# Kernel tuning notes

Measured on AMD Instinct MI355X. Metric: run time of the kernel, lower is better.

The kernel has to match this reference:

```python
import jax, jax.numpy as jnp
import numpy as np

D_K = 128

def setup_inputs() -> dict:
    key = jax.random.key(0)
    k1, k2, k3 = jax.random.split(key, 3)
    q = jax.random.normal(k1, (8192, D_K), dtype=jnp.float32)
    k = jax.random.normal(k2, (8192, D_K), dtype=jnp.float32)
    v = jax.random.normal(k3, (8192, D_K), dtype=jnp.float32)
    return {"q": q, "k": k, "v": v}

def reference(q, k, v):
    # scores: [S_q, S_k]
    scores = jnp.einsum('qd,kd->qk', q, k) / jnp.sqrt(jnp.float32(D_K))
    attn = jax.nn.softmax(scores, axis=-1)  # softmax over keys (torch default last dim)
    return jnp.einsum('qk,kd->qd', attn, v)
```

## Files before the change

### kernel.cpp

```cpp
#include <hip/hip_runtime.h>
#include <math.h>


typedef _Float16 f16x8 __attribute__((ext_vector_type(8)));
typedef float    f32x16 __attribute__((ext_vector_type(16)));

constexpr int S_LEN = 8192;
constexpr int D_K   = 128;
constexpr int NSLICE = 8;
constexpr int ITERS2 = (S_LEN / NSLICE) / 64;

constexpr size_t WS_L_OFF = 0;
constexpr size_t KV_OFF   = 262144;
constexpr size_t PART_OFF = KV_OFF + (size_t)256 * 16384;
constexpr size_t WS_NEED  = PART_OFF + (size_t)7 * S_LEN * D_K * 4;

#define CSCALE (0.08838834764831845f * 1.44269504088896340736f)

union UH8 { _Float16 h[8]; uint4 q; f16x8 v; };
union UF4 { unsigned u[4]; uint4 q; f16x8 v; };

__device__ inline void async16(const uint4* g, uint4* l) {
  __builtin_amdgcn_global_load_lds(
      (const __attribute__((address_space(1))) unsigned int*)g,
      (__attribute__((address_space(3))) unsigned int*)l, 16, 0, 0);
}

template <bool ZOUT>
__global__ __launch_bounds__(512) void attn_prep(const float* __restrict__ K,
                                                 const float* __restrict__ V,
                                                 float* __restrict__ out,
                                                 char* __restrict__ ws) {
  const int t = blockIdx.x * 512 + threadIdx.x;
  uint4* KVg = (uint4*)(ws + KV_OFF);
  if (t < 131072) {
    int kt = t >> 9, idx = t & 511;
    int lane = idx & 63, s = idx >> 6;
    int key = kt * 32 + (lane & 31);
    int d0  = s * 16 + (lane >> 5) * 8;
    const float4* src = (const float4*)(K + (size_t)key * D_K + d0);
    float4 a = src[0], b = src[1];
    float f[8] = {a.x, a.y, a.z, a.w, b.x, b.y, b.z, b.w};
    UH8 h;
    #pragma unroll
    for (int j = 0; j < 8; ++j) h.h[j] = (_Float16)f[j];
    KVg[(size_t)kt * 1024 + idx] = h.q;
  } else if (t < 262144) {
    int g = t - 131072;
    int kt = g >> 9, idx = g & 511;
    int lane = idx & 63, c = (idx >> 6) & 3, kstep = idx >> 8;
    int d  = c * 32 + (lane & 31);
    int kb = kt * 32 + kstep * 16 + (lane >> 5) * 8;
    UH8 h;
    #pragma unroll
    for (int j = 0; j < 8; ++j) h.h[j] = (_Float16)V[(size_t)(kb + j) * D_K + d];
    KVg[(size_t)kt * 1024 + 512 + idx] = h.q;
  } else if (ZOUT && t < 327680) {
    int i = t - 262144;
    float4 z = make_float4(0.f, 0.f, 0.f, 0.f);
    float4* o4 = (float4*)out;
    #pragma unroll
    for (int j = 0; j < 4; ++j) o4[(size_t)i * 4 + j] = z;
  } else if (ZOUT && t < 329728) {
    int i = t - 327680;
    ((float4*)(ws + WS_L_OFF))[i] = make_float4(0.f, 0.f, 0.f, 0.f);
  }
}

__device__ inline void softmax32(const f32x16& Sa, const f32x16& Sb, int lhalf,
                                 float& lsum, UF4& A0, UF4& A1) {
  unsigned pk[8];
  #pragma unroll
  for (int i = 0; i < 8; ++i) {
    float p0 = __builtin_amdgcn_exp2f(Sa[2 * i]     + Sb[2 * i]);
    float p1 = __builtin_amdgcn_exp2f(Sa[2 * i + 1] + Sb[2 * i + 1]);
    lsum += p0 + p1;
    pk[i] = __builtin_bit_cast(unsigned, __builtin_amdgcn_cvt_pkrtz(p0, p1));
  }
  unsigned s0 = __shfl_xor(pk[0], 32), s1 = __shfl_xor(pk[1], 32);
  unsigned s2 = __shfl_xor(pk[2], 32), s3 = __shfl_xor(pk[3], 32);
  unsigned s4 = __shfl_xor(pk[4], 32), s5 = __shfl_xor(pk[5], 32);
  unsigned s6 = __shfl_xor(pk[6], 32), s7 = __shfl_xor(pk[7], 32);
  A0.u[0] = lhalf ? s2 : pk[0];
  A0.u[1] = lhalf ? s3 : pk[1];
  A0.u[2] = lhalf ? pk[2] : s0;
  A0.u[3] = lhalf ? pk[3] : s1;
  A1.u[0] = lhalf ? s6 : pk[4];
  A1.u[1] = lhalf ? s7 : pk[5];
  A1.u[2] = lhalf ? pk[6] : s4;
  A1.u[3] = lhalf ? pk[7] : s5;
}

__device__ inline void pv8(const UF4& A0, const UF4& A1, const f16x8* vf,
                           f32x16* O) {
  #pragma unroll
  for (int kstep = 0; kstep < 2; ++kstep) {
    f16x8 pf = kstep ? A1.v : A0.v;
    O[0] = __builtin_amdgcn_mfma_f32_32x32x16_f16(pf, vf[kstep * 4 + 0], O[0], 0, 0, 0);
    O[1] = __builtin_amdgcn_mfma_f32_32x32x16_f16(pf, vf[kstep * 4 + 1], O[1], 0, 0, 0);
    O[2] = __builtin_amdgcn_mfma_f32_32x32x16_f16(pf, vf[kstep * 4 + 2], O[2], 0, 0, 0);
    O[3] = __builtin_amdgcn_mfma_f32_32x32x16_f16(pf, vf[kstep * 4 + 3], O[3], 0, 0, 0);
  }
}

template <bool PARTIAL>
__global__ __launch_bounds__(128, 1)
void attn_main(const float* __restrict__ Qg, float* __restrict__ out,
               char* __restrict__ ws) {
  __shared__ uint4 KV[2][2048];

  const int tid   = threadIdx.x;
  const int wave  = tid >> 6;
  const int lane  = tid & 63;
  const int lrow  = lane & 31;
  const int lhalf = lane >> 5;

  const int blk = blockIdx.x;
  const int ks  = blk & 7;
  const int qb  = blk >> 3;
  const int qw  = qb * 128 + wave * 64;

  float* ws_l = (float*)(ws + WS_L_OFF);

  f16x8 qf[2][8];
  #pragma unroll
  for (int qt = 0; qt < 2; ++qt) {
    const int q = qw + qt * 32 + lrow;
    #pragma unroll
    for (int s = 0; s < 8; ++s) {
      const float4* src = (const float4*)(Qg + (size_t)q * D_K + s * 16 + lhalf * 8);
      float4 a = src[0], b = src[1];
      float f[8] = {a.x, a.y, a.z, a.w, b.x, b.y, b.z, b.w};
      UH8 h;
      #pragma unroll
      for (int j = 0; j < 8; ++j) h.h[j] = (_Float16)(f[j] * CSCALE);
      qf[qt][s] = h.v;
    }
  }

  f32x16 O0[4] = {f32x16{}, f32x16{}, f32x16{}, f32x16{}};
  f32x16 O1[4] = {f32x16{}, f32x16{}, f32x16{}, f32x16{}};
  float ls0 = 0.f, ls1 = 0.f;

  const uint4* KVg = (const uint4*)(ws + KV_OFF);

  {
    const size_t base = (size_t)ks * 32768;
    #pragma unroll
    for (int i = 0; i < 16; ++i)
      async16(KVg + base + i * 128 + tid, &KV[0][i * 128 + tid]);
  }

  for (int it = 0; it < ITERS2; ++it) {
    const int buf = it & 1;
    __syncthreads();

    if (it + 1 < ITERS2) {
      const size_t base = (size_t)ks * 32768 + (size_t)(it + 1) * 2048;
      #pragma unroll
      for (int i = 0; i < 16; ++i)
        async16(KVg + base + i * 128 + tid, &KV[buf ^ 1][i * 128 + tid]);
    }

    #pragma unroll
    for (int st = 0; st < 2; ++st) {
      const uint4* sub = &KV[buf][st * 1024];

      f16x8 kf[8];
      #pragma unroll
      for (int s = 0; s < 8; ++s)
        kf[s] = __builtin_bit_cast(f16x8, sub[s * 64 + lane]);

      f32x16 Sa0{}, Sb0{}, Sa1{}, Sb1{};
      #pragma unroll
      for (int s = 0; s < 4; ++s) {
        Sa0 = __builtin_amdgcn_mfma_f32_32x32x16_f16(kf[2 * s    ], qf[0][2 * s    ], Sa0, 0, 0, 0);
        Sb0 = __builtin_amdgcn_mfma_f32_32x32x16_f16(kf[2 * s + 1], qf[0][2 * s + 1], Sb0, 0, 0, 0);
      }
      #pragma unroll
      for (int s = 0; s < 4; ++s) {
        Sa1 = __builtin_amdgcn_mfma_f32_32x32x16_f16(kf[2 * s    ], qf[1][2 * s    ], Sa1, 0, 0, 0);
        Sb1 = __builtin_amdgcn_mfma_f32_32x32x16_f16(kf[2 * s + 1], qf[1][2 * s + 1], Sb1, 0, 0, 0);
      }

      f16x8 vf[8];
      #pragma unroll
      for (int i = 0; i < 8; ++i)
        vf[i] = __builtin_bit_cast(f16x8, sub[512 + i * 64 + lane]);

      UF4 A00, A01;
      softmax32(Sa0, Sb0, lhalf, ls0, A00, A01);
      pv8(A00, A01, vf, O0);

      UF4 A10, A11;
      softmax32(Sa1, Sb1, lhalf, ls1, A10, A11);
      pv8(A10, A11, vf, O1);
    }
  }

  ls0 += __shfl_xor(ls0, 32);
  ls1 += __shfl_xor(ls1, 32);

  if (PARTIAL) {
    if (lhalf == 0) {
      ws_l[ks * S_LEN + qw      + lrow] = ls0;
      ws_l[ks * S_LEN + qw + 32 + lrow] = ls1;
    }
    float* obase = (ks == 0) ? out
                 : (float*)(ws + PART_OFF) + (size_t)(ks - 1) * S_LEN * D_K;
    #pragma unroll
    for (int r = 0; r < 16; ++r) {
      int row = (r & 3) + 8 * (r >> 2) + 4 * lhalf;
      float* dst = obase + (size_t)(qw + row) * D_K + lrow;
      dst[ 0] = O0[0][r];
      dst[32] = O0[1][r];
      dst[64] = O0[2][r];
      dst[96] = O0[3][r];
      float* dst1 = obase + (size_t)(qw + 32 + row) * D_K + lrow;
      dst1[ 0] = O1[0][r];
      dst1[32] = O1[1][r];
      dst1[64] = O1[2][r];
      dst1[96] = O1[3][r];
    }
  } else {
    if (lhalf == 0) {
      atomicAdd(ws_l + qw      + lrow, ls0);
      atomicAdd(ws_l + qw + 32 + lrow, ls1);
    }
    #pragma unroll
    for (int r = 0; r < 16; ++r) {
      int row = (r & 3) + 8 * (r >> 2) + 4 * lhalf;
      float* dst = out + (size_t)(qw + row) * D_K + lrow;
      atomicAdd(dst +  0, O0[0][r]);
      atomicAdd(dst + 32, O0[1][r]);
      atomicAdd(dst + 64, O0[2][r]);
      atomicAdd(dst + 96, O0[3][r]);
      float* dst1 = out + (size_t)(qw + 32 + row) * D_K + lrow;
      atomicAdd(dst1 +  0, O1[0][r]);
      atomicAdd(dst1 + 32, O1[1][r]);
      atomicAdd(dst1 + 64, O1[2][r]);
      atomicAdd(dst1 + 96, O1[3][r]);
    }
  }
}

__global__ __launch_bounds__(256) void attn_norm(float* __restrict__ out,
                                                 const float* __restrict__ lpart,
                                                 const float* __restrict__ opart,
                                                 int nparts) {
  int i = blockIdx.x * 256 + threadIdx.x;
  int q = i >> 5;
  float4* o4 = (float4*)out;
  float4 acc = o4[i];
  float l = lpart[q];
  for (int s = 1; s <= nparts; ++s) {
    float4 p = ((const float4*)opart)[(size_t)(s - 1) * 262144 + i];
    acc.x += p.x; acc.y += p.y; acc.z += p.z; acc.w += p.w;
    l += lpart[s * S_LEN + q];
  }
  float inv = 1.0f / l;
  acc.x *= inv; acc.y *= inv; acc.z *= inv; acc.w *= inv;
  o4[i] = acc;
}

extern "C" void kernel_launch(void* const* d_in, const int* in_sizes, int n_in,
                              void* d_out, int out_size, void* d_ws, size_t ws_size,
                              hipStream_t stream) {
  const float* q = (const float*)d_in[0];
  const float* k = (const float*)d_in[1];
  const float* v = (const float*)d_in[2];
  float* out = (float*)d_out;
  char* ws = (char*)d_ws;

  if (ws_size >= WS_NEED) {
    attn_prep<false><<<dim3(512), dim3(512), 0, stream>>>(k, v, out, ws);
    attn_main<true><<<dim3(512), dim3(128), 0, stream>>>(q, out, ws);
    attn_norm<<<dim3(1024), dim3(256), 0, stream>>>(
        out, (const float*)(ws + WS_L_OFF), (const float*)(ws + PART_OFF), 7);
  } else {
    attn_prep<true><<<dim3(645), dim3(512), 0, stream>>>(k, v, out, ws);
    attn_main<false><<<dim3(512), dim3(128), 0, stream>>>(q, out, ws);
    attn_norm<<<dim3(1024), dim3(256), 0, stream>>>(
        out, (const float*)(ws + WS_L_OFF), (const float*)(ws + PART_OFF), 0);
  }
}
```

Measured before the change: 120.8 us.

## Double KV split to 16 slices, 4-wave blocks, permlane swap and setprio

Doubles the key split count to 16 and widens blocks to 4 waves covering 256 queries, so each block shares its KV tile across more waves, with two blocks allowed per CU. It replaces the shfl_xor-based half-wave exchange with permlane32_swap, interleaves the QK MFMAs so K fragments are loaded just in time, and raises wave priority around MFMA sections. In exchange, the merge step must combine twice as many partial outputs, and the workspace grows to match. The zero-output fallback path still relies on the attn_prep zeroing, which may not match the new slice layout.

```diff
diff --git a/kernel.cpp b/kernel.cpp
--- a/kernel.cpp
+++ b/kernel.cpp
@@ -7,13 +7,13 @@
 
 constexpr int S_LEN = 8192;
 constexpr int D_K   = 128;
-constexpr int NSLICE = 8;
+constexpr int NSLICE = 16;
 constexpr int ITERS2 = (S_LEN / NSLICE) / 64;
 
 constexpr size_t WS_L_OFF = 0;
-constexpr size_t KV_OFF   = 262144;
+constexpr size_t KV_OFF   = 524288;
 constexpr size_t PART_OFF = KV_OFF + (size_t)256 * 16384;
-constexpr size_t WS_NEED  = PART_OFF + (size_t)7 * S_LEN * D_K * 4;
+constexpr size_t WS_NEED  = PART_OFF + (size_t)15 * S_LEN * D_K * 4;
 
 #define CSCALE (0.08838834764831845f * 1.44269504088896340736f)
 
@@ -67,7 +67,7 @@
   }
 }
 
-__device__ inline void softmax32(const f32x16& Sa, const f32x16& Sb, int lhalf,
+__device__ inline void softmax32(const f32x16& Sa, const f32x16& Sb,
                                  float& lsum, UF4& A0, UF4& A1) {
   unsigned pk[8];
   #pragma unroll
@@ -77,22 +77,19 @@
     lsum += p0 + p1;
     pk[i] = __builtin_bit_cast(unsigned, __builtin_amdgcn_cvt_pkrtz(p0, p1));
   }
-  unsigned s0 = __shfl_xor(pk[0], 32), s1 = __shfl_xor(pk[1], 32);
-  unsigned s2 = __shfl_xor(pk[2], 32), s3 = __shfl_xor(pk[3], 32);
-  unsigned s4 = __shfl_xor(pk[4], 32), s5 = __shfl_xor(pk[5], 32);
-  unsigned s6 = __shfl_xor(pk[6], 32), s7 = __shfl_xor(pk[7], 32);
-  A0.u[0] = lhalf ? s2 : pk[0];
-  A0.u[1] = lhalf ? s3 : pk[1];
-  A0.u[2] = lhalf ? pk[2] : s0;
-  A0.u[3] = lhalf ? pk[3] : s1;
-  A1.u[0] = lhalf ? s6 : pk[4];
-  A1.u[1] = lhalf ? s7 : pk[5];
-  A1.u[2] = lhalf ? pk[6] : s4;
-  A1.u[3] = lhalf ? pk[7] : s5;
+  auto r0 = __builtin_amdgcn_permlane32_swap((int)pk[0], (int)pk[2], false, false);
+  auto r1 = __builtin_amdgcn_permlane32_swap((int)pk[1], (int)pk[3], false, false);
+  auto r2 = __builtin_amdgcn_permlane32_swap((int)pk[4], (int)pk[6], false, false);
+  auto r3 = __builtin_amdgcn_permlane32_swap((int)pk[5], (int)pk[7], false, false);
+  A0.u[0] = (unsigned)r0[0]; A0.u[2] = (unsigned)r0[1];
+  A0.u[1] = (unsigned)r1[0]; A0.u[3] = (unsigned)r1[1];
+  A1.u[0] = (unsigned)r2[0]; A1.u[2] = (unsigned)r2[1];
+  A1.u[1] = (unsigned)r3[0]; A1.u[3] = (unsigned)r3[1];
 }
 
 __device__ inline void pv8(const UF4& A0, const UF4& A1, const f16x8* vf,
                            f32x16* O) {
+  __builtin_amdgcn_s_setprio(1);
   #pragma unroll
   for (int kstep = 0; kstep < 2; ++kstep) {
     f16x8 pf = kstep ? A1.v : A0.v;
@@ -101,10 +98,11 @@
     O[2] = __builtin_amdgcn_mfma_f32_32x32x16_f16(pf, vf[kstep * 4 + 2], O[2], 0, 0, 0);
     O[3] = __builtin_amdgcn_mfma_f32_32x32x16_f16(pf, vf[kstep * 4 + 3], O[3], 0, 0, 0);
   }
+  __builtin_amdgcn_s_setprio(0);
 }
 
 template <bool PARTIAL>
-__global__ __launch_bounds__(128, 1)
+__global__ __launch_bounds__(256, 2)
 void attn_main(const float* __restrict__ Qg, float* __restrict__ out,
                char* __restrict__ ws) {
   __shared__ uint4 KV[2][2048];
@@ -116,9 +114,9 @@
   const int lhalf = lane >> 5;
 
   const int blk = blockIdx.x;
-  const int ks  = blk & 7;
-  const int qb  = blk >> 3;
-  const int qw  = qb * 128 + wave * 64;
+  const int ks  = blk & 15;
+  const int qb  = blk >> 4;
+  const int qw  = qb * 256 + wave * 64;
 
   float* ws_l = (float*)(ws + WS_L_OFF);
 
@@ -143,45 +141,39 @@
   float ls0 = 0.f, ls1 = 0.f;
 
   const uint4* KVg = (const uint4*)(ws + KV_OFF);
-
-  {
-    const size_t base = (size_t)ks * 32768;
-    #pragma unroll
-    for (int i = 0; i < 16; ++i)
-      async16(KVg + base + i * 128 + tid, &KV[0][i * 128 + tid]);
-  }
+  const size_t sbase = (size_t)ks * 16384;
+
+  #pragma unroll
+  for (int i = 0; i < 8; ++i)
+    async16(KVg + sbase + i * 256 + tid, &KV[0][i * 256 + tid]);
 
   for (int it = 0; it < ITERS2; ++it) {
     const int buf = it & 1;
     __syncthreads();
 
     if (it + 1 < ITERS2) {
-      const size_t base = (size_t)ks * 32768 + (size_t)(it + 1) * 2048;
-      #pragma unroll
-      for (int i = 0; i < 16; ++i)
-        async16(KVg + base + i * 128 + tid, &KV[buf ^ 1][i * 128 + tid]);
+      const size_t base = sbase + (size_t)(it + 1) * 2048;
+      #pragma unroll
+      for (int i = 0; i < 8; ++i)
+        async16(KVg + base + i * 256 + tid, &KV[buf ^ 1][i * 256 + tid]);
     }
 
     #pragma unroll
     for (int st = 0; st < 2; ++st) {
       const uint4* sub = &KV[buf][st * 1024];
 
-      f16x8 kf[8];
-      #pragma unroll
-      for (int s = 0; s < 8; ++s)
-        kf[s] = __builtin_bit_cast(f16x8, sub[s * 64 + lane]);
-
       f32x16 Sa0{}, Sb0{}, Sa1{}, Sb1{};
+      __builtin_amdgcn_s_setprio(1);
       #pragma unroll
       for (int s = 0; s < 4; ++s) {
-        Sa0 = __builtin_amdgcn_mfma_f32_32x32x16_f16(kf[2 * s    ], qf[0][2 * s    ], Sa0, 0, 0, 0);
-        Sb0 = __builtin_amdgcn_mfma_f32_32x32x16_f16(kf[2 * s + 1], qf[0][2 * s + 1], Sb0, 0, 0, 0);
+        f16x8 ka = __builtin_bit_cast(f16x8, sub[(2 * s    ) * 64 + lane]);
+        f16x8 kb = __builtin_bit_cast(f16x8, sub[(2 * s + 1) * 64 + lane]);
+        Sa0 = __builtin_amdgcn_mfma_f32_32x32x16_f16(ka, qf[0][2 * s    ], Sa0, 0, 0, 0);
+        Sa1 = __builtin_amdgcn_mfma_f32_32x32x16_f16(ka, qf[1][2 * s    ], Sa1, 0, 0, 0);
+        Sb0 = __builtin_amdgcn_mfma_f32_32x32x16_f16(kb, qf[0][2 * s + 1], Sb0, 0, 0, 0);
+        Sb1 = __builtin_amdgcn_mfma_f32_32x32x16_f16(kb, qf[1][2 * s + 1], Sb1, 0, 0, 0);
       }
-      #pragma unroll
-      for (int s = 0; s < 4; ++s) {
-        Sa1 = __builtin_amdgcn_mfma_f32_32x32x16_f16(kf[2 * s    ], qf[1][2 * s    ], Sa1, 0, 0, 0);
-        Sb1 = __builtin_amdgcn_mfma_f32_32x32x16_f16(kf[2 * s + 1], qf[1][2 * s + 1], Sb1, 0, 0, 0);
-      }
+      __builtin_amdgcn_s_setprio(0);
 
       f16x8 vf[8];
       #pragma unroll
@@ -189,11 +181,11 @@
         vf[i] = __builtin_bit_cast(f16x8, sub[512 + i * 64 + lane]);
 
       UF4 A00, A01;
-      softmax32(Sa0, Sb0, lhalf, ls0, A00, A01);
+      softmax32(Sa0, Sb0, ls0, A00, A01);
       pv8(A00, A01, vf, O0);
 
       UF4 A10, A11;
-      softmax32(Sa1, Sb1, lhalf, ls1, A10, A11);
+      softmax32(Sa1, Sb1, ls1, A10, A11);
       pv8(A10, A11, vf, O1);
     }
   }
@@ -274,12 +266,12 @@
 
   if (ws_size >= WS_NEED) {
     attn_prep<false><<<dim3(512), dim3(512), 0, stream>>>(k, v, out, ws);
-    attn_main<true><<<dim3(512), dim3(128), 0, stream>>>(q, out, ws);
+    attn_main<true><<<dim3(512), dim3(256), 0, stream>>>(q, out, ws);
     attn_norm<<<dim3(1024), dim3(256), 0, stream>>>(
-        out, (const float*)(ws + WS_L_OFF), (const float*)(ws + PART_OFF), 7);
+        out, (const float*)(ws + WS_L_OFF), (const float*)(ws + PART_OFF), 15);
   } else {
     attn_prep<true><<<dim3(645), dim3(512), 0, stream>>>(k, v, out, ws);
-    attn_main<false><<<dim3(512), dim3(128), 0, stream>>>(q, out, ws);
+    attn_main<false><<<dim3(512), dim3(256), 0, stream>>>(q, out, ws);
     attn_norm<<<dim3(1024), dim3(256), 0, stream>>>(
         out, (const float*)(ws + WS_L_OFF), (const float*)(ws + PART_OFF), 0);
   }
```

Measured after the change: 250.5 us. 107% more time.
